# Kernel tuning notes

Measured on AMD Instinct MI355X. Metric: run time of the kernel, lower is better.

## Reference

```python
import jax, jax.numpy as jnp
import numpy as np

B, N, D_SIM = 4096, 64, 768
NLI_DIM = 768
KK = 5
H1, NUM_CLASSES = 1024, 4


def setup_inputs() -> dict:
    key = jax.random.key(0)
    ks = jax.random.split(key, 8)
    sim_stance_emb = jax.random.normal(ks[0], (B, D_SIM), dtype=jnp.float32)
    nli_stance_emb = jax.random.normal(ks[1], (B, NLI_DIM), dtype=jnp.float32)
    sim_body_emb = jax.random.normal(ks[2], (B, N, D_SIM), dtype=jnp.float32)
    nli_body_emb = jax.random.normal(ks[3], (B, N, NLI_DIM), dtype=jnp.float32)
    fan1 = (KK + 1) * NLI_DIM
    W1 = jax.random.uniform(ks[4], (H1, fan1), jnp.float32, -1.0, 1.0) / jnp.sqrt(fan1)
    b1 = jax.random.uniform(ks[5], (H1,), jnp.float32, -1.0, 1.0) / jnp.sqrt(fan1)
    W2 = jax.random.uniform(ks[6], (NUM_CLASSES, H1), jnp.float32, -1.0, 1.0) / jnp.sqrt(H1)
    b2 = jax.random.uniform(ks[7], (NUM_CLASSES,), jnp.float32, -1.0, 1.0) / jnp.sqrt(H1)
    return {"sim_stance_emb": sim_stance_emb, "nli_stance_emb": nli_stance_emb,
            "sim_body_emb": sim_body_emb, "nli_body_emb": nli_body_emb,
            "W1": W1, "b1": b1, "W2": W2, "b2": b2}


def reference(sim_stance_emb, nli_stance_emb, sim_body_emb, nli_body_emb, W1, b1, W2, b2):
    # sims[b, n] = <sim_stance_emb[b], sim_body_emb[b, n]>  (bmm + squeeze)
    sims = jnp.einsum('bd,bnd->bn', sim_stance_emb, sim_body_emb)
    _, top_idx = jax.lax.top_k(sims, KK)                      # [B, KK]
    # gather top-k nli body sentence embeddings: [B, KK, NLI_DIM]
    top_emb = jnp.take_along_axis(nli_body_emb, top_idx[:, :, None], axis=1)
    xx = jnp.concatenate([nli_stance_emb, top_emb.reshape(top_emb.shape[0], -1)], axis=1)
    xx = jax.nn.relu(xx @ W1.T + b1)
    return xx @ W2.T + b2
```

## Files before the change

### kernel.cpp

```cpp
#include <hip/hip_runtime.h>
#include <stdint.h>
#include <stddef.h>

#define B_N   4096
#define NSENT 64
#define DDIM  768
#define TOPK  5
#define FAN1  4608
#define H1DIM 1024
#define NCLS  4
#define KDIM  4608
#define KHALF 2304

typedef __attribute__((ext_vector_type(8))) __bf16 bf16x8;
typedef __attribute__((ext_vector_type(4))) float  f32x4;

__device__ __forceinline__ unsigned short f2bf(float f) {
    unsigned int u = __float_as_uint(f);
    unsigned int r = (u + 0x7fffu + ((u >> 16) & 1u)) >> 16;
    return (unsigned short)r;
}

__device__ __forceinline__ void gl_lds16(const void* g, void* l) {
    __builtin_amdgcn_global_load_lds((__attribute__((address_space(1))) void*)(g),
                                     (__attribute__((address_space(3))) void*)(l),
                                     16, 0, 0);
}

__global__ __launch_bounds__(256) void k_topk_gather(
    const float* __restrict__ sim_stance,
    const float* __restrict__ sim_body,
    const float* __restrict__ nli_stance,
    const float* __restrict__ nli_body,
    unsigned short* __restrict__ xx)
{
    const int b    = blockIdx.x;
    const int tid  = threadIdx.x;
    const int lane = tid & 63;
    const int wave = tid >> 6;
    const int g    = lane >> 4;
    const int c    = lane & 15;
    __shared__ float sims[NSENT];
    __shared__ int   topidx[TOPK];

    const float4* st4 = (const float4*)(sim_stance + (size_t)b * DDIM);
    float4 st[12];
    #pragma unroll
    for (int j = 0; j < 12; ++j) st[j] = st4[c + 16 * j];

    const float* bodyb = sim_body + (size_t)b * NSENT * DDIM;
    #pragma unroll 1
    for (int it = 0; it < 4; ++it) {
        const int r = wave * 16 + it * 4 + g;
        const float4* r4 = (const float4*)(bodyb + (size_t)r * DDIM);
        float p = 0.f;
        #pragma unroll
        for (int j = 0; j < 12; ++j) {
            float4 v = r4[c + 16 * j];
            p += v.x*st[j].x + v.y*st[j].y + v.z*st[j].z + v.w*st[j].w;
        }
        #pragma unroll
        for (int off = 8; off; off >>= 1) p += __shfl_xor(p, off);
        if (c == 0) sims[r] = p;
    }
    __syncthreads();

    if (wave == 0) {
        float v = sims[lane];
        #pragma unroll
        for (int k = 0; k < TOPK; ++k) {
            float bv = v; int bi = lane;
            #pragma unroll
            for (int off = 32; off; off >>= 1) {
                float ov = __shfl_xor(bv, off);
                int   oi = __shfl_xor(bi, off);
                if (ov > bv || (ov == bv && oi < bi)) { bv = ov; bi = oi; }
            }
            if (lane == 0) topidx[k] = bi;
            if (lane == bi) v = -3.402823466e38f;
        }
    }
    __syncthreads();

    unsigned short* xrow = xx + (size_t)b * FAN1;
    for (int task = tid; task < 1152; task += 256) {
        const int seg = task / 192;
        const int t   = task - seg * 192;
        const float* src = (seg == 0)
            ? (nli_stance + (size_t)b * DDIM)
            : (nli_body + ((size_t)b * NSENT + topidx[seg - 1]) * DDIM);
        float4 v = ((const float4*)src)[t];
        ushort4 o;
        o.x = f2bf(v.x); o.y = f2bf(v.y); o.z = f2bf(v.z); o.w = f2bf(v.w);
        ((ushort4*)(xrow + seg * DDIM))[t] = o;
    }
}

__global__ __launch_bounds__(256) void k_f32_to_bf16x4(
    const float* __restrict__ in, unsigned short* __restrict__ o, int n4)
{
    int i = blockIdx.x * 256 + threadIdx.x;
    if (i < n4) {
        float4 v = ((const float4*)in)[i];
        ushort4 r;
        r.x = f2bf(v.x); r.y = f2bf(v.y); r.z = f2bf(v.z); r.w = f2bf(v.w);
        ((ushort4*)o)[i] = r;
    }
}

__global__ __launch_bounds__(256, 2) void k_gemm1(
    const unsigned short* __restrict__ A,
    const unsigned short* __restrict__ W,
    float* __restrict__ P)
{
    constexpr int BM = 128, BN = 128, BK = 64;
    constexpr int K = KDIM;
    constexpr int NT = KHALF / BK;
    __shared__ unsigned short lA[2][BM * BK];
    __shared__ unsigned short lB[2][BN * BK];

    const int tid = threadIdx.x, lane = tid & 63, wave = tid >> 6;
    const int bid = blockIdx.x;
    const int wk  = (bid & 7) * 64 + (bid >> 3);
    const int ks  = wk >> 8;
    const int rem = wk & 255;
    const int bm  = rem >> 3, bn = rem & 7;
    const int wm = wave >> 1, wn = wave & 1;
    const int k0 = ks * KHALF;

    const int rowq = wave * 8 + (lane >> 3);
    const int sc   = (lane & 7) ^ (lane >> 3);
    const unsigned short* gA[4];
    const unsigned short* gB[4];
    #pragma unroll
    for (int j = 0; j < 4; ++j) {
        gA[j] = A + (size_t)(bm * BM + j * 32 + rowq) * K + k0 + sc * 8;
        gB[j] = W + (size_t)(bn * BN + j * 32 + rowq) * K + k0 + sc * 8;
    }
    const int ldsOff = (wave * 64) * 8;

    const int r16 = lane & 15;
    const int p0  = (lane >> 4) ^ (r16 & 7);
    const int p1  = p0 ^ 4;
    const int aRowOff = (wm * 64 + r16) * BK;
    const int bRowOff = (wn * 64 + r16) * BK;

    f32x4 acc[4][4];
    #pragma unroll
    for (int m = 0; m < 4; ++m)
        #pragma unroll
        for (int n = 0; n < 4; ++n) acc[m][n] = {0.f, 0.f, 0.f, 0.f};

#define STAGE(SEL, T) do {                                                  \
    _Pragma("unroll")                                                       \
    for (int j = 0; j < 4; ++j)                                             \
        gl_lds16(gA[j] + (size_t)(T) * BK, &lA[SEL][j * 2048 + ldsOff]);    \
    _Pragma("unroll")                                                       \
    for (int j = 0; j < 4; ++j)                                             \
        gl_lds16(gB[j] + (size_t)(T) * BK, &lB[SEL][j * 2048 + ldsOff]);    \
} while (0)

#define COMPUTE(SEL) do {                                                   \
    bf16x8 fa[4][2], fb[4][2];                                              \
    _Pragma("unroll")                                                       \
    for (int m = 0; m < 4; ++m) {                                           \
        fa[m][0] = *(const bf16x8*)(&lA[SEL][aRowOff + m * 16 * BK + p0 * 8]); \
        fa[m][1] = *(const bf16x8*)(&lA[SEL][aRowOff + m * 16 * BK + p1 * 8]); \
    }                                                                       \
    _Pragma("unroll")                                                       \
    for (int n = 0; n < 4; ++n) {                                           \
        fb[n][0] = *(const bf16x8*)(&lB[SEL][bRowOff + n * 16 * BK + p0 * 8]); \
        fb[n][1] = *(const bf16x8*)(&lB[SEL][bRowOff + n * 16 * BK + p1 * 8]); \
    }                                                                       \
    _Pragma("unroll")                                                       \
    for (int h = 0; h < 2; ++h)                                             \
        _Pragma("unroll")                                                   \
        for (int m = 0; m < 4; ++m)                                         \
            _Pragma("unroll")                                               \
            for (int n = 0; n < 4; ++n)                                     \
                acc[m][n] = __builtin_amdgcn_mfma_f32_16x16x32_bf16(        \
                    fa[m][h], fb[n][h], acc[m][n], 0, 0, 0);                \
} while (0)

#define SYNCPIPE() asm volatile("s_waitcnt vmcnt(0)\n\ts_barrier" ::: "memory")

    STAGE(0, 0);
    SYNCPIPE();
    #pragma unroll 1
    for (int it = 0; it < 17; ++it) {
        const int t = 2 * it;
        STAGE(1, t + 1); COMPUTE(0); SYNCPIPE();
        STAGE(0, t + 2); COMPUTE(1); SYNCPIPE();
    }
    STAGE(1, 35); COMPUTE(0); SYNCPIPE();
    COMPUTE(1);

#undef STAGE
#undef COMPUTE
#undef SYNCPIPE

    float* Pk = P + (size_t)ks * B_N * H1DIM;
    const int colbase = bn * BN + wn * 64 + r16;
    const int rowbase = bm * BM + wm * 64 + (lane >> 4) * 4;
    #pragma unroll
    for (int n = 0; n < 4; ++n) {
        const int col = colbase + n * 16;
        #pragma unroll
        for (int m = 0; m < 4; ++m) {
            const int row = rowbase + m * 16;
            #pragma unroll
            for (int j = 0; j < 4; ++j)
                Pk[(size_t)(row + j) * H1DIM + col] = acc[m][n][j];
        }
    }
}

__global__ __launch_bounds__(256) void k_gemm2(
    const float* __restrict__ P, const float* __restrict__ W2,
    const float* __restrict__ b1, const float* __restrict__ b2,
    float* __restrict__ out)
{
    __shared__ float w2s[NCLS * H1DIM + H1DIM];
    const int tid = threadIdx.x, lane = tid & 63, wave = tid >> 6;
    const int row = blockIdx.x * 4 + wave;
    for (int i = tid; i < NCLS * H1DIM; i += 256) w2s[i] = W2[i];
    for (int i = tid; i < H1DIM; i += 256) w2s[NCLS * H1DIM + i] = b1[i];
    __syncthreads();

    const float4* p0 = (const float4*)(P + (size_t)row * H1DIM);
    const float4* p1 = (const float4*)(P + (size_t)(B_N + row) * H1DIM);
    const float4* w0 = (const float4*)&w2s[0];
    const float4* w1 = (const float4*)&w2s[H1DIM];
    const float4* w2 = (const float4*)&w2s[2 * H1DIM];
    const float4* w3 = (const float4*)&w2s[3 * H1DIM];
    const float4* bb = (const float4*)&w2s[4 * H1DIM];
    float a0 = 0.f, a1 = 0.f, a2 = 0.f, a3 = 0.f;
    #pragma unroll
    for (int j = 0; j < 4; ++j) {
        const int idx = j * 64 + lane;
        float4 x0 = p0[idx], x1 = p1[idx], bv = bb[idx];
        float4 h;
        h.x = x0.x + x1.x + bv.x; h.x = h.x > 0.f ? h.x : 0.f;
        h.y = x0.y + x1.y + bv.y; h.y = h.y > 0.f ? h.y : 0.f;
        h.z = x0.z + x1.z + bv.z; h.z = h.z > 0.f ? h.z : 0.f;
        h.w = x0.w + x1.w + bv.w; h.w = h.w > 0.f ? h.w : 0.f;
        float4 xv;
        xv = w0[idx]; a0 += h.x*xv.x + h.y*xv.y + h.z*xv.z + h.w*xv.w;
        xv = w1[idx]; a1 += h.x*xv.x + h.y*xv.y + h.z*xv.z + h.w*xv.w;
        xv = w2[idx]; a2 += h.x*xv.x + h.y*xv.y + h.z*xv.z + h.w*xv.w;
        xv = w3[idx]; a3 += h.x*xv.x + h.y*xv.y + h.z*xv.z + h.w*xv.w;
    }
    #pragma unroll
    for (int off = 32; off; off >>= 1) {
        a0 += __shfl_xor(a0, off);
        a1 += __shfl_xor(a1, off);
        a2 += __shfl_xor(a2, off);
        a3 += __shfl_xor(a3, off);
    }
    if (lane == 0) {
        float* o = out + (size_t)row * NCLS;
        o[0] = a0 + b2[0]; o[1] = a1 + b2[1]; o[2] = a2 + b2[2]; o[3] = a3 + b2[3];
    }
}

extern "C" void kernel_launch(void* const* d_in, const int* in_sizes, int n_in,
                              void* d_out, int out_size, void* d_ws, size_t ws_size,
                              hipStream_t stream)
{
    const float* sim_stance = (const float*)d_in[0];
    const float* nli_stance = (const float*)d_in[1];
    const float* sim_body   = (const float*)d_in[2];
    const float* nli_body   = (const float*)d_in[3];
    const float* W1 = (const float*)d_in[4];
    const float* b1 = (const float*)d_in[5];
    const float* W2 = (const float*)d_in[6];
    const float* b2 = (const float*)d_in[7];
    float* out = (float*)d_out;

    char* ws = (char*)d_ws;
    unsigned short* xx  = (unsigned short*)ws;
    unsigned short* w1b = (unsigned short*)(ws + 37748736u);
    float*          P   = (float*)(ws + 37748736u + 9437184u);

    k_f32_to_bf16x4<<<dim3(4608), dim3(256), 0, stream>>>(W1, w1b, 1179648);
    k_topk_gather<<<dim3(B_N), dim3(256), 0, stream>>>(sim_stance, sim_body,
                                                       nli_stance, nli_body, xx);
    k_gemm1<<<dim3(512), dim3(256), 0, stream>>>(xx, w1b, P);
    k_gemm2<<<dim3(1024), dim3(256), 0, stream>>>(P, W2, b1, b2, out);
}
```

Baseline: 257.3 us.

## Map one batch row per wave in topk-gather kernel, removing block barriers

The top-k/gather kernel now assigns one batch row to each wave, with four rows per block, instead of one row per 256-thread block. Each wave computes all 64 similarities, runs its own shuffle-based top-5 and gathers its row, so both __syncthreads barriers go away and the other waves no longer idle during selection. The cost is less memory-level parallelism per row and more serial loop iterations per wave. The step reads about 800 MB of sim_body, so it is likely bandwidth-bound and the change may matter little.

```diff
diff --git a/kernel.cpp b/kernel.cpp
--- a/kernel.cpp
+++ b/kernel.cpp
@@ -27,21 +27,20 @@
                                      16, 0, 0);
 }
 
-__global__ __launch_bounds__(256) void k_topk_gather(
+__global__ __launch_bounds__(256, 4) void k_topk_gather(
     const float* __restrict__ sim_stance,
     const float* __restrict__ sim_body,
     const float* __restrict__ nli_stance,
     const float* __restrict__ nli_body,
     unsigned short* __restrict__ xx)
 {
-    const int b    = blockIdx.x;
     const int tid  = threadIdx.x;
     const int lane = tid & 63;
     const int wave = tid >> 6;
+    const int b    = blockIdx.x * 4 + wave;
     const int g    = lane >> 4;
     const int c    = lane & 15;
-    __shared__ float sims[NSENT];
-    __shared__ int   topidx[TOPK];
+    __shared__ float sims_s[4][NSENT];
 
     const float4* st4 = (const float4*)(sim_stance + (size_t)b * DDIM);
     float4 st[12];
@@ -50,8 +49,8 @@
 
     const float* bodyb = sim_body + (size_t)b * NSENT * DDIM;
     #pragma unroll 1
-    for (int it = 0; it < 4; ++it) {
-        const int r = wave * 16 + it * 4 + g;
+    for (int it = 0; it < 16; ++it) {
+        const int r = it * 4 + g;
         const float4* r4 = (const float4*)(bodyb + (size_t)r * DDIM);
         float p = 0.f;
         #pragma unroll
@@ -61,38 +60,38 @@
         }
         #pragma unroll
         for (int off = 8; off; off >>= 1) p += __shfl_xor(p, off);
-        if (c == 0) sims[r] = p;
-    }
-    __syncthreads();
-
-    if (wave == 0) {
-        float v = sims[lane];
-        #pragma unroll
-        for (int k = 0; k < TOPK; ++k) {
-            float bv = v; int bi = lane;
-            #pragma unroll
-            for (int off = 32; off; off >>= 1) {
-                float ov = __shfl_xor(bv, off);
-                int   oi = __shfl_xor(bi, off);
-                if (ov > bv || (ov == bv && oi < bi)) { bv = ov; bi = oi; }
-            }
-            if (lane == 0) topidx[k] = bi;
-            if (lane == bi) v = -3.402823466e38f;
-        }
-    }
-    __syncthreads();
+        if (c == 0) sims_s[wave][r] = p;
+    }
+
+    float v = sims_s[wave][lane];
+    int topidx[TOPK];
+    #pragma unroll
+    for (int k = 0; k < TOPK; ++k) {
+        float bv = v; int bi = lane;
+        #pragma unroll
+        for (int off = 32; off; off >>= 1) {
+            float ov = __shfl_xor(bv, off);
+            int   oi = __shfl_xor(bi, off);
+            if (ov > bv || (ov == bv && oi < bi)) { bv = ov; bi = oi; }
+        }
+        topidx[k] = bi;
+        if (lane == bi) v = -3.402823466e38f;
+    }
 
     unsigned short* xrow = xx + (size_t)b * FAN1;
-    for (int task = tid; task < 1152; task += 256) {
-        const int seg = task / 192;
-        const int t   = task - seg * 192;
+    #pragma unroll
+    for (int seg = 0; seg < 6; ++seg) {
         const float* src = (seg == 0)
             ? (nli_stance + (size_t)b * DDIM)
             : (nli_body + ((size_t)b * NSENT + topidx[seg - 1]) * DDIM);
-        float4 v = ((const float4*)src)[t];
-        ushort4 o;
-        o.x = f2bf(v.x); o.y = f2bf(v.y); o.z = f2bf(v.z); o.w = f2bf(v.w);
-        ((ushort4*)(xrow + seg * DDIM))[t] = o;
+        #pragma unroll
+        for (int t = 0; t < 3; ++t) {
+            const int i = t * 64 + lane;
+            float4 vv = ((const float4*)src)[i];
+            ushort4 o;
+            o.x = f2bf(vv.x); o.y = f2bf(vv.y); o.z = f2bf(vv.z); o.w = f2bf(vv.w);
+            ((ushort4*)(xrow + seg * DDIM))[i] = o;
+        }
     }
 }
 
@@ -115,7 +114,6 @@
 {
     constexpr int BM = 128, BN = 128, BK = 64;
     constexpr int K = KDIM;
-    constexpr int NT = KHALF / BK;
     __shared__ unsigned short lA[2][BM * BK];
     __shared__ unsigned short lB[2][BN * BK];
 
@@ -283,8 +281,8 @@
     float*          P   = (float*)(ws + 37748736u + 9437184u);
 
     k_f32_to_bf16x4<<<dim3(4608), dim3(256), 0, stream>>>(W1, w1b, 1179648);
-    k_topk_gather<<<dim3(B_N), dim3(256), 0, stream>>>(sim_stance, sim_body,
-                                                       nli_stance, nli_body, xx);
+    k_topk_gather<<<dim3(1024), dim3(256), 0, stream>>>(sim_stance, sim_body,
+                                                        nli_stance, nli_body, xx);
     k_gemm1<<<dim3(512), dim3(256), 0, stream>>>(xx, w1b, P);
     k_gemm2<<<dim3(1024), dim3(256), 0, stream>>>(P, W2, b1, b2, out);
 }
```

Result: faster. 247.0 us (-4.0%).
